# Optimization experiments

Hardware: AMD Instinct MI355X
Metric: run time of the kernel (lower is better)

Reference implementation:

```python
import jax, jax.numpy as jnp
import numpy as np

EPS = 1e-7
NUM_ROUTING = 3


def squash(s, axis=-1):
    # v = ||s||^2/(1+||s||^2) * s/||s||, numerically safe
    sq = jnp.sum(jnp.square(s), axis=axis, keepdims=True)
    scale = sq / (1.0 + sq) / jnp.sqrt(sq + EPS)
    return scale * s


def setup_inputs() -> dict:
    key = jax.random.key(0)
    k1, k2 = jax.random.split(key)
    B, IN_CAPS, IN_DIM = 256, 1152, 8
    NUM_CAPS, DIM_VEC = 10, 16
    inputs = jax.random.normal(k1, (B, IN_CAPS, IN_DIM), dtype=jnp.float32)
    # glorot_uniform over [in_caps, num_caps, dim_vec, in_dim]
    limit = np.sqrt(6.0 / (IN_DIM + DIM_VEC))
    W = jax.random.uniform(k2, (IN_CAPS, NUM_CAPS, DIM_VEC, IN_DIM), dtype=jnp.float32,
                           minval=-limit, maxval=limit)
    bias = jnp.zeros((IN_CAPS, NUM_CAPS), dtype=jnp.float32)
    return {"inputs": inputs, "W": W, "bias": bias}


def reference(inputs, W, bias):
    # u_hat[b,i,c,d] = W[i,c,d,e] @ inputs[b,i,e]
    u_hat = jnp.einsum('icde,bie->bicd', W, inputs)  # [B, in_caps, num_caps, dim_vec]
    b = bias[None]  # [1, in_caps, num_caps], broadcasts to [B, ...]
    for _ in range(NUM_ROUTING - 1):
        c = jax.nn.softmax(b, axis=2)                       # over num_capsule
        s = jnp.einsum('bic,bicd->bcd', c * jnp.ones_like(u_hat[..., 0]), u_hat)
        v = squash(s, axis=-1)                              # [B, num_caps, dim_vec]
        agreement = jnp.einsum('bicd,bcd->bic', u_hat, v)
        b = agreement + b + bias[None]
    c_last = jax.nn.softmax(b, axis=2)
    s = jnp.einsum('bic,bicd->bcd', c_last * jnp.ones_like(u_hat[..., 0]), u_hat)
    outputs = squash(s, axis=-1)                            # [B, num_caps, dim_vec]
    return outputs
```

## Files before the change

kernel.cpp:

```cpp
#include <hip/hip_runtime.h>
#include <math.h>

#define BATCH 256
#define IC    1152
#define EDIM  8
#define NC    10
#define DV    16

#define ITILE 8
#define NB    16
#define NTHREADS 256
#define NWAVES 4
#define ICHUNKS (IC / ITILE)
#define BCHUNKS (BATCH / NB)
#define SCD (NC * DV)
#define SPART_STRIDE (BATCH * SCD)

template<int CTRL>
__device__ __forceinline__ float dpp_add(float x) {
    int r = __builtin_amdgcn_update_dpp(0, __float_as_int(x), CTRL, 0xF, 0xF, true);
    return x + __int_as_float(r);
}
__device__ __forceinline__ float row_reduce16(float x) {
    x = dpp_add<0xB1>(x);
    x = dpp_add<0x4E>(x);
    x = dpp_add<0x141>(x);
    x = dpp_add<0x140>(x);
    return x;
}

template<int MODE>
__global__ __launch_bounds__(NTHREADS)
void caps_main(const float* __restrict__ x,
               const float* __restrict__ W,
               const float* __restrict__ bias,
               const float* __restrict__ v_in,
               float* __restrict__ b2,
               float* __restrict__ s_part)
{
    __shared__ float sx[NB][ITILE * EDIM];
    __shared__ float swv[NWAVES][NB][SCD];

    const int tid = threadIdx.x;
    const int d   = tid & 15;
    const int ch  = (tid >> 4) & 1;
    const int il  = tid >> 5;
    const int wid = tid >> 6;
    const int icb = blockIdx.x;
    const int bcb = blockIdx.y;
    const int i0  = icb * ITILE;
    const int b0  = bcb * NB;
    const int i   = i0 + il;

    {
        const float4* xg = (const float4*)x;
        float4* xs = (float4*)&sx[0][0];
        int bb = tid >> 4;
        int w  = tid & 15;
        xs[tid] = xg[(size_t)(b0 + bb) * (IC * EDIM / 4) + i0 * (EDIM / 4) + w];
    }

    float4 w4[5][2];
    float  bv[5];
    const float4* Wg = (const float4*)W;
    #pragma unroll
    for (int k = 0; k < 5; ++k) {
        int c = ch * 5 + k;
        size_t base = ((size_t)(i * NC + c) * DV + d) * 2;
        w4[k][0] = Wg[base];
        w4[k][1] = Wg[base + 1];
        bv[k]    = bias[i * NC + c];
    }

    float cw[5];
    if (MODE == 1) {
        float mx = fmaxf(fmaxf(fmaxf(bv[0], bv[1]), fmaxf(bv[2], bv[3])), bv[4]);
        mx = fmaxf(mx, __shfl_xor(mx, 16));
        float ssum = 0.f, ex[5];
        #pragma unroll
        for (int k = 0; k < 5; ++k) { ex[k] = __expf(bv[k] - mx); ssum += ex[k]; }
        ssum += __shfl_xor(ssum, 16);
        float inv = 1.0f / ssum;
        #pragma unroll
        for (int k = 0; k < 5; ++k) cw[k] = ex[k] * inv;
    }

    __syncthreads();

    #pragma unroll 2
    for (int bb = 0; bb < NB; ++bb) {
        const int b = b0 + bb;
        const float4 x0 = ((const float4*)&sx[bb][il * EDIM])[0];
        const float4 x1 = ((const float4*)&sx[bb][il * EDIM])[1];

        float u[5];
        #pragma unroll
        for (int k = 0; k < 5; ++k) {
            float acc = w4[k][0].x * x0.x;
            acc = fmaf(w4[k][0].y, x0.y, acc);
            acc = fmaf(w4[k][0].z, x0.z, acc);
            acc = fmaf(w4[k][0].w, x0.w, acc);
            acc = fmaf(w4[k][1].x, x1.x, acc);
            acc = fmaf(w4[k][1].y, x1.y, acc);
            acc = fmaf(w4[k][1].z, x1.z, acc);
            acc = fmaf(w4[k][1].w, x1.w, acc);
            u[k] = acc;
        }

        if (MODE != 1) {
            const float* vb = v_in + (size_t)b * SCD + ch * 80 + d;
            float t[5];
            #pragma unroll
            for (int k = 0; k < 5; ++k) t[k] = u[k] * vb[k * 16];
            #pragma unroll
            for (int k = 0; k < 5; ++k) t[k] = row_reduce16(t[k]);

            float br[5];
            if (MODE == 2) {
                #pragma unroll
                for (int k = 0; k < 5; ++k) br[k] = t[k] + 2.0f * bv[k];
                if (d == 0) {
                    float* bp = b2 + ((size_t)b * IC + i) * NC + ch * 5;
                    #pragma unroll
                    for (int k = 0; k < 5; ++k) bp[k] = br[k];
                }
            } else {
                const float* bp = b2 + ((size_t)b * IC + i) * NC + ch * 5;
                #pragma unroll
                for (int k = 0; k < 5; ++k) br[k] = t[k] + bp[k] + bv[k];
            }
            float mx = fmaxf(fmaxf(fmaxf(br[0], br[1]), fmaxf(br[2], br[3])), br[4]);
            mx = fmaxf(mx, __shfl_xor(mx, 16));
            float ssum = 0.f, ex[5];
            #pragma unroll
            for (int k = 0; k < 5; ++k) { ex[k] = __expf(br[k] - mx); ssum += ex[k]; }
            ssum += __shfl_xor(ssum, 16);
            float inv = 1.0f / ssum;
            #pragma unroll
            for (int k = 0; k < 5; ++k) cw[k] = ex[k] * inv;
        }

        float sval[5];
        #pragma unroll
        for (int k = 0; k < 5; ++k) sval[k] = cw[k] * u[k];
        #pragma unroll
        for (int k = 0; k < 5; ++k) sval[k] += __shfl_xor(sval[k], 32);
        if ((tid & 32) == 0) {
            #pragma unroll
            for (int k = 0; k < 5; ++k)
                swv[wid][bb][ch * 80 + k * 16 + d] = sval[k];
        }
    }

    __syncthreads();

    #pragma unroll
    for (int r = 0; r < (NB * SCD) / NTHREADS; ++r) {
        int j  = tid + r * NTHREADS;
        int bb = j / SCD;
        int cd = j - bb * SCD;
        float s = (swv[0][bb][cd] + swv[1][bb][cd])
                + (swv[2][bb][cd] + swv[3][bb][cd]);
        s_part[((size_t)icb * BATCH + b0 + bb) * SCD + cd] = s;
    }
}

__global__ __launch_bounds__(256)
void caps_squash(const float* __restrict__ s_part, float* __restrict__ out)
{
    const int tid = threadIdx.x;
    const int bc  = blockIdx.x * 16 + (tid >> 4);
    const size_t off = (size_t)bc * DV + (tid & 15);

    float a[8] = {0.f, 0.f, 0.f, 0.f, 0.f, 0.f, 0.f, 0.f};
    #pragma unroll 2
    for (int ic = 0; ic < ICHUNKS; ic += 8) {
        #pragma unroll
        for (int j = 0; j < 8; ++j)
            a[j] += s_part[(size_t)(ic + j) * SPART_STRIDE + off];
    }
    float s = ((a[0] + a[1]) + (a[2] + a[3])) + ((a[4] + a[5]) + (a[6] + a[7]));

    float sq = row_reduce16(s * s);

    float scale = sq / ((1.0f + sq) * sqrtf(sq + 1e-7f));
    out[off] = scale * s;
}

extern "C" void kernel_launch(void* const* d_in, const int* in_sizes, int n_in,
                              void* d_out, int out_size, void* d_ws, size_t ws_size,
                              hipStream_t stream)
{
    const float* x    = (const float*)d_in[0];
    const float* W    = (const float*)d_in[1];
    const float* bias = (const float*)d_in[2];
    float* out = (float*)d_out;

    float* ws     = (float*)d_ws;
    float* s_part = ws;
    float* v      = s_part + (size_t)ICHUNKS * SPART_STRIDE;
    float* b2     = v + SPART_STRIDE;

    dim3 grid(ICHUNKS, BCHUNKS);

    caps_main<1><<<grid, NTHREADS, 0, stream>>>(x, W, bias, v, b2, s_part);
    caps_squash<<<160, 256, 0, stream>>>(s_part, v);
    caps_main<2><<<grid, NTHREADS, 0, stream>>>(x, W, bias, v, b2, s_part);
    caps_squash<<<160, 256, 0, stream>>>(s_part, v);
    caps_main<3><<<grid, NTHREADS, 0, stream>>>(x, W, bias, v, b2, s_part);
    caps_squash<<<160, 256, 0, stream>>>(s_part, out);
}
```

Baseline: 203.8 us.

## Accumulate s partials in registers over multiple input-capsule chunks per block

Each block now loops over four 8-capsule chunks (32 input capsules) with a smaller batch tile of 8, keeping per-thread s accumulators in registers. Partial sums are written to shared memory and global memory once at the end instead of per batch element. This cuts the s_part slab count by four, which shrinks the cross-chunk reduction in the squash kernel and the global write traffic. In exchange the block holds more registers for sacc, a launch-bounds occupancy hint is added, the grid has fewer blocks, and W is reused across fewer batch elements per load.

```diff
diff --git a/kernel.cpp b/kernel.cpp
--- a/kernel.cpp
+++ b/kernel.cpp
@@ -7,11 +7,13 @@
 #define NC    10
 #define DV    16
 
-#define ITILE 8
-#define NB    16
+#define ITILE  8
+#define NCHUNK 4
+#define ITOT   (ITILE * NCHUNK)
+#define NB     8
 #define NTHREADS 256
 #define NWAVES 4
-#define ICHUNKS (IC / ITILE)
+#define NSLAB  (IC / ITOT)
 #define BCHUNKS (BATCH / NB)
 #define SCD (NC * DV)
 #define SPART_STRIDE (BATCH * SCD)
@@ -30,7 +32,7 @@
 }
 
 template<int MODE>
-__global__ __launch_bounds__(NTHREADS)
+__global__ __launch_bounds__(NTHREADS, 4)
 void caps_main(const float* __restrict__ x,
                const float* __restrict__ W,
                const float* __restrict__ bias,
@@ -38,7 +40,7 @@
                float* __restrict__ b2,
                float* __restrict__ s_part)
 {
-    __shared__ float sx[NB][ITILE * EDIM];
+    __shared__ float sx[NB][ITOT * EDIM];
     __shared__ float swv[NWAVES][NB][SCD];
 
     const int tid = threadIdx.x;
@@ -48,112 +50,127 @@
     const int wid = tid >> 6;
     const int icb = blockIdx.x;
     const int bcb = blockIdx.y;
-    const int i0  = icb * ITILE;
+    const int i0  = icb * ITOT;
     const int b0  = bcb * NB;
-    const int i   = i0 + il;
 
     {
         const float4* xg = (const float4*)x;
         float4* xs = (float4*)&sx[0][0];
-        int bb = tid >> 4;
-        int w  = tid & 15;
-        xs[tid] = xg[(size_t)(b0 + bb) * (IC * EDIM / 4) + i0 * (EDIM / 4) + w];
-    }
-
-    float4 w4[5][2];
-    float  bv[5];
+        #pragma unroll
+        for (int f = tid; f < NB * ITOT * EDIM / 4; f += NTHREADS) {
+            int bb = f >> 6;
+            int w  = f & 63;
+            xs[f] = xg[(size_t)(b0 + bb) * (IC * EDIM / 4) + i0 * (EDIM / 4) + w];
+        }
+    }
+
+    float sacc[NB][5];
+    #pragma unroll
+    for (int bb = 0; bb < NB; ++bb)
+        #pragma unroll
+        for (int k = 0; k < 5; ++k) sacc[bb][k] = 0.f;
+
+    __syncthreads();
+
     const float4* Wg = (const float4*)W;
-    #pragma unroll
-    for (int k = 0; k < 5; ++k) {
-        int c = ch * 5 + k;
-        size_t base = ((size_t)(i * NC + c) * DV + d) * 2;
-        w4[k][0] = Wg[base];
-        w4[k][1] = Wg[base + 1];
-        bv[k]    = bias[i * NC + c];
-    }
-
-    float cw[5];
-    if (MODE == 1) {
-        float mx = fmaxf(fmaxf(fmaxf(bv[0], bv[1]), fmaxf(bv[2], bv[3])), bv[4]);
-        mx = fmaxf(mx, __shfl_xor(mx, 16));
-        float ssum = 0.f, ex[5];
-        #pragma unroll
-        for (int k = 0; k < 5; ++k) { ex[k] = __expf(bv[k] - mx); ssum += ex[k]; }
-        ssum += __shfl_xor(ssum, 16);
-        float inv = 1.0f / ssum;
-        #pragma unroll
-        for (int k = 0; k < 5; ++k) cw[k] = ex[k] * inv;
-    }
-
-    __syncthreads();
-
-    #pragma unroll 2
-    for (int bb = 0; bb < NB; ++bb) {
-        const int b = b0 + bb;
-        const float4 x0 = ((const float4*)&sx[bb][il * EDIM])[0];
-        const float4 x1 = ((const float4*)&sx[bb][il * EDIM])[1];
-
-        float u[5];
+
+    #pragma unroll 1
+    for (int ic = 0; ic < NCHUNK; ++ic) {
+        const int i = i0 + ic * ITILE + il;
+
+        float4 w4[5][2];
+        float  bv[5];
         #pragma unroll
         for (int k = 0; k < 5; ++k) {
-            float acc = w4[k][0].x * x0.x;
-            acc = fmaf(w4[k][0].y, x0.y, acc);
-            acc = fmaf(w4[k][0].z, x0.z, acc);
-            acc = fmaf(w4[k][0].w, x0.w, acc);
-            acc = fmaf(w4[k][1].x, x1.x, acc);
-            acc = fmaf(w4[k][1].y, x1.y, acc);
-            acc = fmaf(w4[k][1].z, x1.z, acc);
-            acc = fmaf(w4[k][1].w, x1.w, acc);
-            u[k] = acc;
-        }
-
-        if (MODE != 1) {
-            const float* vb = v_in + (size_t)b * SCD + ch * 80 + d;
-            float t[5];
-            #pragma unroll
-            for (int k = 0; k < 5; ++k) t[k] = u[k] * vb[k * 16];
-            #pragma unroll
-            for (int k = 0; k < 5; ++k) t[k] = row_reduce16(t[k]);
-
-            float br[5];
-            if (MODE == 2) {
-                #pragma unroll
-                for (int k = 0; k < 5; ++k) br[k] = t[k] + 2.0f * bv[k];
-                if (d == 0) {
-                    float* bp = b2 + ((size_t)b * IC + i) * NC + ch * 5;
-                    #pragma unroll
-                    for (int k = 0; k < 5; ++k) bp[k] = br[k];
-                }
-            } else {
-                const float* bp = b2 + ((size_t)b * IC + i) * NC + ch * 5;
-                #pragma unroll
-                for (int k = 0; k < 5; ++k) br[k] = t[k] + bp[k] + bv[k];
-            }
-            float mx = fmaxf(fmaxf(fmaxf(br[0], br[1]), fmaxf(br[2], br[3])), br[4]);
+            int c = ch * 5 + k;
+            size_t base = ((size_t)(i * NC + c) * DV + d) * 2;
+            w4[k][0] = Wg[base];
+            w4[k][1] = Wg[base + 1];
+            bv[k]    = bias[i * NC + c];
+        }
+
+        float cw[5];
+        if (MODE == 1) {
+            float mx = fmaxf(fmaxf(fmaxf(bv[0], bv[1]), fmaxf(bv[2], bv[3])), bv[4]);
             mx = fmaxf(mx, __shfl_xor(mx, 16));
             float ssum = 0.f, ex[5];
             #pragma unroll
-            for (int k = 0; k < 5; ++k) { ex[k] = __expf(br[k] - mx); ssum += ex[k]; }
+            for (int k = 0; k < 5; ++k) { ex[k] = __expf(bv[k] - mx); ssum += ex[k]; }
             ssum += __shfl_xor(ssum, 16);
             float inv = 1.0f / ssum;
             #pragma unroll
             for (int k = 0; k < 5; ++k) cw[k] = ex[k] * inv;
         }
 
-        float sval[5];
-        #pragma unroll
-        for (int k = 0; k < 5; ++k) sval[k] = cw[k] * u[k];
-        #pragma unroll
-        for (int k = 0; k < 5; ++k) sval[k] += __shfl_xor(sval[k], 32);
-        if ((tid & 32) == 0) {
+        #pragma unroll
+        for (int bb = 0; bb < NB; ++bb) {
+            const int b = b0 + bb;
+            const float4 x0 = ((const float4*)&sx[bb][(ic * ITILE + il) * EDIM])[0];
+            const float4 x1 = ((const float4*)&sx[bb][(ic * ITILE + il) * EDIM])[1];
+
+            float u[5];
+            #pragma unroll
+            for (int k = 0; k < 5; ++k) {
+                float acc = w4[k][0].x * x0.x;
+                acc = fmaf(w4[k][0].y, x0.y, acc);
+                acc = fmaf(w4[k][0].z, x0.z, acc);
+                acc = fmaf(w4[k][0].w, x0.w, acc);
+                acc = fmaf(w4[k][1].x, x1.x, acc);
+                acc = fmaf(w4[k][1].y, x1.y, acc);
+                acc = fmaf(w4[k][1].z, x1.z, acc);
+                acc = fmaf(w4[k][1].w, x1.w, acc);
+                u[k] = acc;
+            }
+
+            if (MODE != 1) {
+                const float* vb = v_in + (size_t)b * SCD + ch * 80 + d;
+                float t[5];
+                #pragma unroll
+                for (int k = 0; k < 5; ++k) t[k] = u[k] * vb[k * 16];
+                #pragma unroll
+                for (int k = 0; k < 5; ++k) t[k] = row_reduce16(t[k]);
+
+                float br[5];
+                if (MODE == 2) {
+                    #pragma unroll
+                    for (int k = 0; k < 5; ++k) br[k] = t[k] + 2.0f * bv[k];
+                    if (d == 0) {
+                        float* bp = b2 + ((size_t)b * IC + i) * NC + ch * 5;
+                        #pragma unroll
+                        for (int k = 0; k < 5; ++k) bp[k] = br[k];
+                    }
+                } else {
+                    const float* bp = b2 + ((size_t)b * IC + i) * NC + ch * 5;
+                    #pragma unroll
+                    for (int k = 0; k < 5; ++k) br[k] = t[k] + bp[k] + bv[k];
+                }
+                float mx = fmaxf(fmaxf(fmaxf(br[0], br[1]), fmaxf(br[2], br[3])), br[4]);
+                mx = fmaxf(mx, __shfl_xor(mx, 16));
+                float ssum = 0.f, ex[5];
+                #pragma unroll
+                for (int k = 0; k < 5; ++k) { ex[k] = __expf(br[k] - mx); ssum += ex[k]; }
+                ssum += __shfl_xor(ssum, 16);
+                float inv = 1.0f / ssum;
+                #pragma unroll
+                for (int k = 0; k < 5; ++k) cw[k] = ex[k] * inv;
+            }
+
             #pragma unroll
             for (int k = 0; k < 5; ++k)
-                swv[wid][bb][ch * 80 + k * 16 + d] = sval[k];
-        }
-    }
-
+                sacc[bb][k] = fmaf(cw[k], u[k], sacc[bb][k]);
+        }
+    }
+
+    #pragma unroll
+    for (int bb = 0; bb < NB; ++bb) {
+        #pragma unroll
+        for (int k = 0; k < 5; ++k) {
+            float s = sacc[bb][k] + __shfl_xor(sacc[bb][k], 32);
+            if ((tid & 32) == 0)
+                swv[wid][bb][ch * 80 + k * 16 + d] = s;
+        }
+    }
     __syncthreads();
-
     #pragma unroll
     for (int r = 0; r < (NB * SCD) / NTHREADS; ++r) {
         int j  = tid + r * NTHREADS;
@@ -172,14 +189,14 @@
     const int bc  = blockIdx.x * 16 + (tid >> 4);
     const size_t off = (size_t)bc * DV + (tid & 15);
 
-    float a[8] = {0.f, 0.f, 0.f, 0.f, 0.f, 0.f, 0.f, 0.f};
-    #pragma unroll 2
-    for (int ic = 0; ic < ICHUNKS; ic += 8) {
-        #pragma unroll
-        for (int j = 0; j < 8; ++j)
+    float a[4] = {0.f, 0.f, 0.f, 0.f};
+    #pragma unroll
+    for (int ic = 0; ic < NSLAB; ic += 4) {
+        #pragma unroll
+        for (int j = 0; j < 4; ++j)
             a[j] += s_part[(size_t)(ic + j) * SPART_STRIDE + off];
     }
-    float s = ((a[0] + a[1]) + (a[2] + a[3])) + ((a[4] + a[5]) + (a[6] + a[7]));
+    float s = (a[0] + a[1]) + (a[2] + a[3]);
 
     float sq = row_reduce16(s * s);
 
@@ -198,10 +215,10 @@
 
     float* ws     = (float*)d_ws;
     float* s_part = ws;
-    float* v      = s_part + (size_t)ICHUNKS * SPART_STRIDE;
+    float* v      = s_part + (size_t)NSLAB * SPART_STRIDE;
     float* b2     = v + SPART_STRIDE;
 
-    dim3 grid(ICHUNKS, BCHUNKS);
+    dim3 grid(NSLAB, BCHUNKS);
 
     caps_main<1><<<grid, NTHREADS, 0, stream>>>(x, W, bias, v, b2, s_part);
     caps_squash<<<160, 256, 0, stream>>>(s_part, v);
```

After: 448.0 us. 120% more time.
